# Kernel tuning notes

Hardware: AMD Instinct MI355X
Metric: run time of the kernel (lower is better)

The kernel has to match this reference:

```python
import jax, jax.numpy as jnp
import numpy as np

HIDDEN = 2048
NUM_HEADS = 16
HEAD_DIM = 128
BLOCK_SIZE = 64
NUM_ACTIVE_BLOCKS = 4  # diagonal pattern -> bandwidth = 2 blocks each side
NEG_INF = -1e30  # stand-in for -inf that is safe under softmax in fp32


def _block_diagonal_additive_mask(seq_len: int) -> jnp.ndarray:
    """Token-level additive mask [S, S]; 0 where block |bi-bj|<=bandwidth, -inf else."""
    bandwidth = NUM_ACTIVE_BLOCKS // 2
    bid = jnp.arange(seq_len) // BLOCK_SIZE  # [S]
    active = jnp.abs(bid[:, None] - bid[None, :]) <= bandwidth  # [S, S] bool
    return jnp.where(active, 0.0, NEG_INF).astype(jnp.float32)


def setup_inputs() -> dict:
    key = jax.random.key(0)
    k0, k1, k2, k3, k4 = jax.random.split(key, 5)
    B, S = 2, 2048
    scale = 1.0 / np.sqrt(HIDDEN)
    return {
        "hidden_states": jax.random.normal(k0, (B, S, HIDDEN), dtype=jnp.float32),
        "Wq": jax.random.normal(k1, (HIDDEN, NUM_HEADS * HEAD_DIM), dtype=jnp.float32) * scale,
        "Wk": jax.random.normal(k2, (HIDDEN, NUM_HEADS * HEAD_DIM), dtype=jnp.float32) * scale,
        "Wv": jax.random.normal(k3, (HIDDEN, NUM_HEADS * HEAD_DIM), dtype=jnp.float32) * scale,
        "Wo": jax.random.normal(k4, (NUM_HEADS * HEAD_DIM, HIDDEN), dtype=jnp.float32) * scale,
    }


def reference(hidden_states, Wq, Wk, Wv, Wo):
    B, S, _ = hidden_states.shape
    scaling = HEAD_DIM ** -0.5

    # projections -> [B, H, S, D]
    def split_heads(x):
        return x.reshape(B, S, NUM_HEADS, HEAD_DIM).transpose(0, 2, 1, 3)

    q = split_heads(hidden_states @ Wq)
    k = split_heads(hidden_states @ Wk)
    v = split_heads(hidden_states @ Wv)

    mask = _block_diagonal_additive_mask(S)  # [S, S]

    # scores [B, H, S, S]
    scores = jnp.einsum("bhsd,bhtd->bhst", q, k) * scaling + mask[None, None]
    attn = jax.nn.softmax(scores.astype(jnp.float32), axis=-1).astype(q.dtype)

    out = jnp.einsum("bhst,bhtd->bhsd", attn, v)  # [B, H, S, D]
    out = out.transpose(0, 2, 1, 3).reshape(B, S, NUM_HEADS * HEAD_DIM)
    return out @ Wo
```

## Files before the change

kernel.cpp:

```cpp
#include <hip/hip_runtime.h>

typedef __attribute__((ext_vector_type(4))) float f32x4;
typedef __attribute__((ext_vector_type(16))) float f32x16;
typedef __attribute__((ext_vector_type(8))) _Float16 f16x8;
typedef __attribute__((ext_vector_type(4))) _Float16 f16x4;

__device__ __forceinline__ void gload_lds16(const void* g, void* l) {
  __builtin_amdgcn_global_load_lds((__attribute__((address_space(1))) void*)(g),
                                   (__attribute__((address_space(3))) void*)(l), 16, 0, 0);
}

__global__ __launch_bounds__(256) void cast_f32_f16(const float* __restrict__ x,
                                                    _Float16* __restrict__ y, int n) {
  int i = (blockIdx.x * 256 + threadIdx.x) * 4;
  if (i < n) {
    float4 v = *(const float4*)(x + i);
    f16x4 o = { (_Float16)v.x, (_Float16)v.y, (_Float16)v.z, (_Float16)v.w };
    *(f16x4*)(y + i) = o;
  }
}

__global__ __launch_bounds__(256) void wtrans(const float* __restrict__ W0, const float* __restrict__ W1,
                                              const float* __restrict__ W2, const float* __restrict__ W3,
                                              _Float16* __restrict__ out) {
  const float* W = blockIdx.z == 0 ? W0 : blockIdx.z == 1 ? W1 : blockIdx.z == 2 ? W2 : W3;
  _Float16* Wt = out + (size_t)blockIdx.z * (2048u * 2048u);
  __shared__ _Float16 tile[64][65];
  const int tid = threadIdx.x;
  const int k0 = blockIdx.y * 64, n0 = blockIdx.x * 64;
  #pragma unroll
  for (int p = 0; p < 4; ++p) {
    int o = p * 256 + tid, r = o >> 4, c = o & 15;
    float4 v = *(const float4*)(W + (size_t)(k0 + r) * 2048 + n0 + c * 4);
    tile[r][c * 4 + 0] = (_Float16)v.x;
    tile[r][c * 4 + 1] = (_Float16)v.y;
    tile[r][c * 4 + 2] = (_Float16)v.z;
    tile[r][c * 4 + 3] = (_Float16)v.w;
  }
  __syncthreads();
  #pragma unroll
  for (int p = 0; p < 2; ++p) {
    int o = p * 256 + tid, nl = o >> 3, c = o & 7;
    f16x8 u;
    #pragma unroll
    for (int i = 0; i < 8; ++i) u[i] = tile[c * 8 + i][nl];
    *(f16x8*)(Wt + (size_t)(n0 + nl) * 2048 + k0 + c * 8) = u;
  }
}

template <typename OutT>
__global__ __launch_bounds__(256) void gemm_bt(const _Float16* __restrict__ A,
                                               const _Float16* __restrict__ Bt,
                                               OutT* __restrict__ C,
                                               int K, int N, size_t zsB, size_t zsC) {
  Bt += (size_t)blockIdx.z * zsB;
  C  += (size_t)blockIdx.z * zsC;
  __shared__ _Float16 As[128 * 64];
  __shared__ _Float16 Bs[128 * 64];
  const int tid = threadIdx.x;
  const int m0 = blockIdx.y * 128, n0 = blockIdx.x * 128;
  const int lane = tid & 63, w = tid >> 6, l32 = lane & 31, half = lane >> 5;
  const int wm = (w & 1) * 64, wn = (w >> 1) * 64;
  f32x16 acc[2][2];
  #pragma unroll
  for (int i = 0; i < 2; ++i)
    #pragma unroll
    for (int j = 0; j < 2; ++j) acc[i][j] = 0;

  for (int k0 = 0; k0 < K; k0 += 64) {
    __syncthreads();
    #pragma unroll
    for (int p = 0; p < 4; ++p) {
      int o = p * 256 + tid, r = o >> 3, c = o & 7;
      int cs = ((c ^ (r & 7)) * 8);
      gload_lds16(A  + (size_t)(m0 + r) * K + k0 + cs, (char*)As + o * 16);
      gload_lds16(Bt + (size_t)(n0 + r) * K + k0 + cs, (char*)Bs + o * 16);
    }
    __builtin_amdgcn_s_waitcnt(0);
    __syncthreads();
    #pragma unroll
    for (int kk = 0; kk < 4; ++kk) {
      const int slot = ((2 * kk + half) ^ (l32 & 7)) * 8;
      f16x8 af[2], bf[2];
      #pragma unroll
      for (int s = 0; s < 2; ++s) {
        af[s] = *(const f16x8*)(As + (wm + s * 32 + l32) * 64 + slot);
        bf[s] = *(const f16x8*)(Bs + (wn + s * 32 + l32) * 64 + slot);
      }
      #pragma unroll
      for (int sm = 0; sm < 2; ++sm)
        #pragma unroll
        for (int sn = 0; sn < 2; ++sn)
          acc[sm][sn] = __builtin_amdgcn_mfma_f32_32x32x16_f16(bf[sn], af[sm], acc[sm][sn], 0, 0, 0);
    }
  }
  #pragma unroll
  for (int sm = 0; sm < 2; ++sm) {
    const size_t row = (size_t)(m0 + wm + sm * 32 + l32);
    #pragma unroll
    for (int sn = 0; sn < 2; ++sn) {
      #pragma unroll
      for (int g = 0; g < 4; ++g) {
        const int col = n0 + wn + sn * 32 + g * 8 + 4 * half;
        if constexpr (sizeof(OutT) == 2) {
          f16x4 o = { (_Float16)acc[sm][sn][4 * g + 0], (_Float16)acc[sm][sn][4 * g + 1],
                      (_Float16)acc[sm][sn][4 * g + 2], (_Float16)acc[sm][sn][4 * g + 3] };
          *(f16x4*)((_Float16*)C + row * N + col) = o;
        } else {
          f32x4 o = { acc[sm][sn][4 * g + 0], acc[sm][sn][4 * g + 1],
                      acc[sm][sn][4 * g + 2], acc[sm][sn][4 * g + 3] };
          *(f32x4*)((float*)C + row * N + col) = o;
        }
      }
    }
  }
}

__global__ __launch_bounds__(256) void attn(const _Float16* __restrict__ Qg,
                                            const _Float16* __restrict__ Kg,
                                            const _Float16* __restrict__ Vtg,
                                            _Float16* __restrict__ Og) {
  const int t = blockIdx.x, h = blockIdx.y, b = blockIdx.z;
  __shared__ _Float16 Qs[128 * 128];
  __shared__ _Float16 Ks[64 * 128];
  __shared__ _Float16 Vs[128 * 64];
  const int tid = threadIdx.x;
  const int lane = tid & 63, w = tid >> 6, l16 = lane & 15, quad = lane >> 4;
  const int qbw = 2 * t + (w >> 1);
  const char* QsB = (const char*)Qs;
  const char* KsB = (const char*)Ks;
  const char* VsB = (const char*)Vs;

  #pragma unroll
  for (int p = 0; p < 8; ++p) {
    int o = p * 256 + tid, r = o >> 4, c = o & 15;
    gload_lds16(Qg + (size_t)(b * 2048 + t * 128 + r) * 2048 + h * 128 + ((c ^ (r & 15)) * 8),
                (char*)Qs + o * 16);
  }
  __builtin_amdgcn_s_waitcnt(0);
  __syncthreads();
  f16x8 qf[2][4];
  #pragma unroll
  for (int qc = 0; qc < 2; ++qc)
    #pragma unroll
    for (int ks = 0; ks < 4; ++ks)
      qf[qc][ks] = *(const f16x8*)(QsB + (w * 32 + qc * 16 + l16) * 256 +
                                   (((ks * 4 + quad) ^ l16) * 16));

  const float scale = 0.08838834764831845f;
  float m_[2] = {-1e30f, -1e30f}, l_[2] = {0.f, 0.f};
  f32x4 oacc[8][2];
  #pragma unroll
  for (int dt = 0; dt < 8; ++dt)
    #pragma unroll
    for (int qc = 0; qc < 2; ++qc) oacc[dt][qc] = (f32x4){0.f, 0.f, 0.f, 0.f};

  for (int jj = 0; jj < 6; ++jj) {
    const int j = 2 * t - 2 + jj;
    const int jc = j < 0 ? 0 : (j > 31 ? 31 : j);
    __syncthreads();
    #pragma unroll
    for (int p = 0; p < 4; ++p) {
      int o = p * 256 + tid, r = o >> 4, c = o & 15;
      gload_lds16(Kg + (size_t)(b * 2048 + jc * 64 + r) * 2048 + h * 128 + ((c ^ (r & 15)) * 8),
                  (char*)Ks + o * 16);
    }
    #pragma unroll
    for (int p = 0; p < 4; ++p) {
      int o = p * 256 + tid, d = o >> 3, c = o & 7;
      gload_lds16(Vtg + (size_t)(h * 128 + d) * 4096 + b * 2048 + jc * 64 + ((c ^ (d & 7)) * 8),
                  (char*)Vs + o * 16);
    }
    __builtin_amdgcn_s_waitcnt(0);
    __syncthreads();

    const bool valid = (j >= 0) && (j <= 31) && (j >= qbw - 2) && (j <= qbw + 2);
    if (valid) {
      f32x4 sc[4][2];
      #pragma unroll
      for (int kt = 0; kt < 4; ++kt)
        #pragma unroll
        for (int qc = 0; qc < 2; ++qc) sc[kt][qc] = (f32x4){0.f, 0.f, 0.f, 0.f};
      #pragma unroll
      for (int kt = 0; kt < 4; ++kt)
        #pragma unroll
        for (int ks = 0; ks < 4; ++ks) {
          f16x8 kf = *(const f16x8*)(KsB + (kt * 16 + l16) * 256 + (((ks * 4 + quad) ^ l16) * 16));
          #pragma unroll
          for (int qc = 0; qc < 2; ++qc)
            sc[kt][qc] = __builtin_amdgcn_mfma_f32_16x16x32_f16(kf, qf[qc][ks], sc[kt][qc], 0, 0, 0);
        }
      #pragma unroll
      for (int qc = 0; qc < 2; ++qc) {
        float mj = -1e30f;
        #pragma unroll
        for (int kt = 0; kt < 4; ++kt)
          #pragma unroll
          for (int r = 0; r < 4; ++r) {
            float v = sc[kt][qc][r] * scale;
            sc[kt][qc][r] = v;
            mj = fmaxf(mj, v);
          }
        mj = fmaxf(mj, __shfl_xor(mj, 16));
        mj = fmaxf(mj, __shfl_xor(mj, 32));
        const float mn = fmaxf(m_[qc], mj);
        const float alpha = __expf(m_[qc] - mn);
        float s_ = 0.f;
        #pragma unroll
        for (int kt = 0; kt < 4; ++kt)
          #pragma unroll
          for (int r = 0; r < 4; ++r) {
            float p = __expf(sc[kt][qc][r] - mn);
            sc[kt][qc][r] = p;
            s_ += p;
          }
        s_ += __shfl_xor(s_, 16);
        s_ += __shfl_xor(s_, 32);
        l_[qc] = l_[qc] * alpha + s_;
        m_[qc] = mn;
        #pragma unroll
        for (int dt = 0; dt < 8; ++dt) oacc[dt][qc] *= alpha;
      }
      #pragma unroll
      for (int kt = 0; kt < 4; ++kt) {
        f16x4 pb[2];
        #pragma unroll
        for (int qc = 0; qc < 2; ++qc)
          pb[qc] = (f16x4){ (_Float16)sc[kt][qc][0], (_Float16)sc[kt][qc][1],
                            (_Float16)sc[kt][qc][2], (_Float16)sc[kt][qc][3] };
        #pragma unroll
        for (int dt = 0; dt < 8; ++dt) {
          f16x4 vv = *(const f16x4*)(VsB + (dt * 16 + l16) * 128 +
                                     (((2 * kt + (quad >> 1)) ^ (l16 & 7)) * 16) + (quad & 1) * 8);
          #pragma unroll
          for (int qc = 0; qc < 2; ++qc)
            oacc[dt][qc] = __builtin_amdgcn_mfma_f32_16x16x16f16(vv, pb[qc], oacc[dt][qc], 0, 0, 0);
        }
      }
    }
  }

  #pragma unroll
  for (int qc = 0; qc < 2; ++qc) {
    const float pinv = 1.0f / l_[qc];
    const size_t orow = (size_t)(b * 2048 + t * 128 + w * 32 + qc * 16 + l16);
    #pragma unroll
    for (int dt = 0; dt < 8; ++dt) {
      f16x4 ov = { (_Float16)(oacc[dt][qc][0] * pinv), (_Float16)(oacc[dt][qc][1] * pinv),
                   (_Float16)(oacc[dt][qc][2] * pinv), (_Float16)(oacc[dt][qc][3] * pinv) };
      *(f16x4*)(Og + orow * 2048 + h * 128 + dt * 16 + quad * 4) = ov;
    }
  }
}

extern "C" void kernel_launch(void* const* d_in, const int* in_sizes, int n_in,
                              void* d_out, int out_size, void* d_ws, size_t ws_size,
                              hipStream_t stream) {
  const float* Hs = (const float*)d_in[0];
  const float* Wq = (const float*)d_in[1];
  const float* Wk = (const float*)d_in[2];
  const float* Wv = (const float*)d_in[3];
  const float* Wo = (const float*)d_in[4];
  _Float16* Hb  = (_Float16*)d_ws;
  _Float16* Wt  = Hb  + 8388608;
  _Float16* Qb  = Wt  + 16777216;
  _Float16* Kb  = Qb  + 8388608;
  _Float16* Vtb = Kb  + 8388608;
  _Float16* Ob  = Vtb + 8388608;
  float* out = (float*)d_out;

  cast_f32_f16<<<8192, 256, 0, stream>>>(Hs, Hb, 8388608);
  wtrans<<<dim3(32, 32, 4), 256, 0, stream>>>(Wq, Wk, Wv, Wo, Wt);
  gemm_bt<_Float16><<<dim3(16, 32, 2), 256, 0, stream>>>(Hb, Wt, Qb, 2048, 2048,
                                                         (size_t)4194304, (size_t)8388608);
  gemm_bt<_Float16><<<dim3(32, 16, 1), 256, 0, stream>>>(Wt + 2 * 4194304, Hb, Vtb, 2048, 4096,
                                                         (size_t)0, (size_t)0);
  attn<<<dim3(16, 16, 2), 256, 0, stream>>>(Qb, Kb, Vtb, Ob);
  gemm_bt<float><<<dim3(16, 32, 1), 256, 0, stream>>>(Ob, Wt + 3 * 4194304, out, 2048, 2048,
                                                      (size_t)0, (size_t)0);
}
```

Measured before the change: 363.8 us.

## Merge prep kernels and QKV GEMMs, enlarge GEMM tiles to 256x128

Merges the hidden-state cast and the weight transpose into one prep launch, and merges the Q/K projection and the V-transpose projection into one launch. The combined QKV launch uses larger 256x128 and 128x256 tiles and launch bounds of two blocks per CU. The aim is to cut launch count and tail effects and to raise operand reuse per tile. The cost is more registers and LDS per block and fewer blocks in the grid, which may lower occupancy.

```diff
diff --git a/kernel.cpp b/kernel.cpp
--- a/kernel.cpp
+++ b/kernel.cpp
@@ -10,24 +10,23 @@
                                    (__attribute__((address_space(3))) void*)(l), 16, 0, 0);
 }
 
-__global__ __launch_bounds__(256) void cast_f32_f16(const float* __restrict__ x,
-                                                    _Float16* __restrict__ y, int n) {
-  int i = (blockIdx.x * 256 + threadIdx.x) * 4;
-  if (i < n) {
-    float4 v = *(const float4*)(x + i);
+__global__ __launch_bounds__(256) void prep(const float* __restrict__ Hs,
+                                            const float* __restrict__ W0, const float* __restrict__ W1,
+                                            const float* __restrict__ W2, const float* __restrict__ W3,
+                                            _Float16* __restrict__ Hb, _Float16* __restrict__ Wt) {
+  __shared__ _Float16 tile[64][65];
+  const int bid = blockIdx.x, tid = threadIdx.x;
+  if (bid < 8192) {
+    int i = (bid * 256 + tid) * 4;
+    float4 v = *(const float4*)(Hs + i);
     f16x4 o = { (_Float16)v.x, (_Float16)v.y, (_Float16)v.z, (_Float16)v.w };
-    *(f16x4*)(y + i) = o;
-  }
-}
-
-__global__ __launch_bounds__(256) void wtrans(const float* __restrict__ W0, const float* __restrict__ W1,
-                                              const float* __restrict__ W2, const float* __restrict__ W3,
-                                              _Float16* __restrict__ out) {
-  const float* W = blockIdx.z == 0 ? W0 : blockIdx.z == 1 ? W1 : blockIdx.z == 2 ? W2 : W3;
-  _Float16* Wt = out + (size_t)blockIdx.z * (2048u * 2048u);
-  __shared__ _Float16 tile[64][65];
-  const int tid = threadIdx.x;
-  const int k0 = blockIdx.y * 64, n0 = blockIdx.x * 64;
+    *(f16x4*)(Hb + i) = o;
+    return;
+  }
+  const int t = bid - 8192;
+  const int z = t >> 10, k0 = ((t >> 5) & 31) * 64, n0 = (t & 31) * 64;
+  const float* W = z == 0 ? W0 : z == 1 ? W1 : z == 2 ? W2 : W3;
+  _Float16* Wo_ = Wt + (size_t)z * (2048u * 2048u);
   #pragma unroll
   for (int p = 0; p < 4; ++p) {
     int o = p * 256 + tid, r = o >> 4, c = o & 15;
@@ -44,76 +43,100 @@
     f16x8 u;
     #pragma unroll
     for (int i = 0; i < 8; ++i) u[i] = tile[c * 8 + i][nl];
-    *(f16x8*)(Wt + (size_t)(n0 + nl) * 2048 + k0 + c * 8) = u;
-  }
-}
-
-template <typename OutT>
-__global__ __launch_bounds__(256) void gemm_bt(const _Float16* __restrict__ A,
-                                               const _Float16* __restrict__ Bt,
-                                               OutT* __restrict__ C,
-                                               int K, int N, size_t zsB, size_t zsC) {
-  Bt += (size_t)blockIdx.z * zsB;
-  C  += (size_t)blockIdx.z * zsC;
-  __shared__ _Float16 As[128 * 64];
-  __shared__ _Float16 Bs[128 * 64];
+    *(f16x8*)(Wo_ + (size_t)(n0 + nl) * 2048 + k0 + c * 8) = u;
+  }
+}
+
+template <int SM, int SN, typename OutT>
+__device__ __forceinline__ void gemm_tile(const _Float16* __restrict__ A,
+                                          const _Float16* __restrict__ Bt,
+                                          OutT* __restrict__ C,
+                                          int K, int N, int m0, int n0, _Float16* S) {
+  _Float16* As = S;
+  _Float16* Bs = S + SM * 64 * 64;
   const int tid = threadIdx.x;
-  const int m0 = blockIdx.y * 128, n0 = blockIdx.x * 128;
   const int lane = tid & 63, w = tid >> 6, l32 = lane & 31, half = lane >> 5;
-  const int wm = (w & 1) * 64, wn = (w >> 1) * 64;
-  f32x16 acc[2][2];
-  #pragma unroll
-  for (int i = 0; i < 2; ++i)
-    #pragma unroll
-    for (int j = 0; j < 2; ++j) acc[i][j] = 0;
+  const int wm = (w & 1) * SM * 32, wn = (w >> 1) * SN * 32;
+  f32x16 acc[SM][SN];
+  #pragma unroll
+  for (int s = 0; s < SM; ++s)
+    #pragma unroll
+    for (int t = 0; t < SN; ++t) acc[s][t] = 0;
 
   for (int k0 = 0; k0 < K; k0 += 64) {
     __syncthreads();
     #pragma unroll
-    for (int p = 0; p < 4; ++p) {
+    for (int p = 0; p < SM * 2; ++p) {
       int o = p * 256 + tid, r = o >> 3, c = o & 7;
-      int cs = ((c ^ (r & 7)) * 8);
-      gload_lds16(A  + (size_t)(m0 + r) * K + k0 + cs, (char*)As + o * 16);
-      gload_lds16(Bt + (size_t)(n0 + r) * K + k0 + cs, (char*)Bs + o * 16);
+      gload_lds16(A + (size_t)(m0 + r) * K + k0 + ((c ^ (r & 7)) * 8), (char*)As + o * 16);
+    }
+    #pragma unroll
+    for (int p = 0; p < SN * 2; ++p) {
+      int o = p * 256 + tid, r = o >> 3, c = o & 7;
+      gload_lds16(Bt + (size_t)(n0 + r) * K + k0 + ((c ^ (r & 7)) * 8), (char*)Bs + o * 16);
     }
     __builtin_amdgcn_s_waitcnt(0);
     __syncthreads();
     #pragma unroll
     for (int kk = 0; kk < 4; ++kk) {
       const int slot = ((2 * kk + half) ^ (l32 & 7)) * 8;
-      f16x8 af[2], bf[2];
-      #pragma unroll
-      for (int s = 0; s < 2; ++s) {
-        af[s] = *(const f16x8*)(As + (wm + s * 32 + l32) * 64 + slot);
-        bf[s] = *(const f16x8*)(Bs + (wn + s * 32 + l32) * 64 + slot);
-      }
-      #pragma unroll
-      for (int sm = 0; sm < 2; ++sm)
-        #pragma unroll
-        for (int sn = 0; sn < 2; ++sn)
-          acc[sm][sn] = __builtin_amdgcn_mfma_f32_32x32x16_f16(bf[sn], af[sm], acc[sm][sn], 0, 0, 0);
-    }
-  }
-  #pragma unroll
-  for (int sm = 0; sm < 2; ++sm) {
-    const size_t row = (size_t)(m0 + wm + sm * 32 + l32);
-    #pragma unroll
-    for (int sn = 0; sn < 2; ++sn) {
+      f16x8 af[SM], bf[SN];
+      #pragma unroll
+      for (int s = 0; s < SM; ++s) af[s] = *(const f16x8*)(As + (wm + s * 32 + l32) * 64 + slot);
+      #pragma unroll
+      for (int t = 0; t < SN; ++t) bf[t] = *(const f16x8*)(Bs + (wn + t * 32 + l32) * 64 + slot);
+      #pragma unroll
+      for (int s = 0; s < SM; ++s)
+        #pragma unroll
+        for (int t = 0; t < SN; ++t)
+          acc[s][t] = __builtin_amdgcn_mfma_f32_32x32x16_f16(bf[t], af[s], acc[s][t], 0, 0, 0);
+    }
+  }
+  #pragma unroll
+  for (int s = 0; s < SM; ++s) {
+    const size_t row = (size_t)(m0 + wm + s * 32 + l32);
+    #pragma unroll
+    for (int t = 0; t < SN; ++t) {
       #pragma unroll
       for (int g = 0; g < 4; ++g) {
-        const int col = n0 + wn + sn * 32 + g * 8 + 4 * half;
+        const int col = n0 + wn + t * 32 + g * 8 + 4 * half;
         if constexpr (sizeof(OutT) == 2) {
-          f16x4 o = { (_Float16)acc[sm][sn][4 * g + 0], (_Float16)acc[sm][sn][4 * g + 1],
-                      (_Float16)acc[sm][sn][4 * g + 2], (_Float16)acc[sm][sn][4 * g + 3] };
+          f16x4 o = { (_Float16)acc[s][t][4 * g + 0], (_Float16)acc[s][t][4 * g + 1],
+                      (_Float16)acc[s][t][4 * g + 2], (_Float16)acc[s][t][4 * g + 3] };
           *(f16x4*)((_Float16*)C + row * N + col) = o;
         } else {
-          f32x4 o = { acc[sm][sn][4 * g + 0], acc[sm][sn][4 * g + 1],
-                      acc[sm][sn][4 * g + 2], acc[sm][sn][4 * g + 3] };
+          f32x4 o = { acc[s][t][4 * g + 0], acc[s][t][4 * g + 1],
+                      acc[s][t][4 * g + 2], acc[s][t][4 * g + 3] };
           *(f32x4*)((float*)C + row * N + col) = o;
         }
       }
     }
   }
+}
+
+__global__ __launch_bounds__(256, 2) void qkvv(const _Float16* __restrict__ Hb,
+                                               const _Float16* __restrict__ Wt,
+                                               _Float16* __restrict__ Qb,
+                                               _Float16* __restrict__ Vtb) {
+  __shared__ _Float16 S[24576];
+  const int id = blockIdx.x;
+  if (id < 512) {
+    const int z = id >> 8, t = id & 255;
+    gemm_tile<4, 2>(Hb, Wt + (size_t)z * 4194304, Qb + (size_t)z * 8388608,
+                    2048, 2048, (t >> 4) * 256, (t & 15) * 128, S);
+  } else {
+    const int t = id - 512;
+    gemm_tile<2, 4>(Wt + (size_t)2 * 4194304, Hb, Vtb,
+                    2048, 4096, (t >> 4) * 128, (t & 15) * 256, S);
+  }
+}
+
+__global__ __launch_bounds__(256) void gemm_wo(const _Float16* __restrict__ A,
+                                               const _Float16* __restrict__ Bt,
+                                               float* __restrict__ C) {
+  __shared__ _Float16 S[16384];
+  const int t = blockIdx.x;
+  gemm_tile<2, 2>(A, Bt, C, 2048, 2048, (t >> 4) * 128, (t & 15) * 128, S);
 }
 
 __global__ __launch_bounds__(256) void attn(const _Float16* __restrict__ Qg,
@@ -268,14 +291,10 @@
   _Float16* Vtb = Kb  + 8388608;
   _Float16* Ob  = Vtb + 8388608;
   float* out = (float*)d_out;
-
-  cast_f32_f16<<<8192, 256, 0, stream>>>(Hs, Hb, 8388608);
-  wtrans<<<dim3(32, 32, 4), 256, 0, stream>>>(Wq, Wk, Wv, Wo, Wt);
-  gemm_bt<_Float16><<<dim3(16, 32, 2), 256, 0, stream>>>(Hb, Wt, Qb, 2048, 2048,
-                                                         (size_t)4194304, (size_t)8388608);
-  gemm_bt<_Float16><<<dim3(32, 16, 1), 256, 0, stream>>>(Wt + 2 * 4194304, Hb, Vtb, 2048, 4096,
-                                                         (size_t)0, (size_t)0);
+  (void)Kb;
+
+  prep<<<12288, 256, 0, stream>>>(Hs, Wq, Wk, Wv, Wo, Hb, Wt);
+  qkvv<<<768, 256, 0, stream>>>(Hb, Wt, Qb, Vtb);
   attn<<<dim3(16, 16, 2), 256, 0, stream>>>(Qb, Kb, Vtb, Ob);
-  gemm_bt<float><<<dim3(16, 32, 1), 256, 0, stream>>>(Ob, Wt + 3 * 4194304, out, 2048, 2048,
-                                                      (size_t)0, (size_t)0);
-}
+  gemm_wo<<<512, 256, 0, stream>>>(Ob, Wt + (size_t)3 * 4194304, out);
+}
```

New measurement: 349.3 us. 4.0% less time.
